# Kernel optimization log

Hardware: AMD Instinct MI355X
Metric: run time of the kernel (lower is better)

Reference implementation:

```python
import jax, jax.numpy as jnp
import numpy as np

N_NODES = 100000
N_EDGES = 1600000
D = 64
N_LAYERS = 5


def setup_inputs() -> dict:
    key = jax.random.key(0)
    k1, k2, k3, k4 = jax.random.split(key, 4)
    x = jax.random.normal(k1, (N_NODES, D), dtype=jnp.float32)
    edge_index = jax.random.randint(k2, (2, N_EDGES), 0, N_NODES, dtype=jnp.int32)
    scale = 1.0 / np.sqrt(D)
    Wl = jax.random.normal(k3, (N_LAYERS, D, D), dtype=jnp.float32) * scale
    Wr = jax.random.normal(k4, (N_LAYERS, D, D), dtype=jnp.float32) * scale
    b = jnp.zeros((N_LAYERS, D), dtype=jnp.float32)
    return {"x": x, "edge_index": edge_index, "Wl": Wl, "Wr": Wr, "b": b}


def reference(x, edge_index, Wl, Wr, b):
    # PyG SAGEConv (mean aggr): out = lin_l(mean_{j->i} x_j) + lin_r(x_i)
    # bias lives on lin_l; messages flow src=edge_index[0] -> dst=edge_index[1].
    src = edge_index[0]
    dst = edge_index[1]
    n = x.shape[0]
    deg = jax.ops.segment_sum(jnp.ones((src.shape[0],), x.dtype), dst, num_segments=n)
    inv_deg = (1.0 / jnp.maximum(deg, 1.0))[:, None]  # [N,1]

    def conv(h, i):
        agg = jax.ops.segment_sum(h[src], dst, num_segments=n) * inv_deg  # [N,D] mean of neighbors
        return agg @ Wl[i] + b[i] + h @ Wr[i]

    # first num_layers-1 convs with relu (+ residual for i>0); dropout is identity in eval mode
    for i in range(N_LAYERS - 1):
        prev = x
        x = conv(x, i)
        if i > 0:
            x = x + prev
        x = jax.nn.relu(x)
    return conv(x, N_LAYERS - 1)
```

## Files before the change

### kernel.cpp

```cpp
#include <hip/hip_runtime.h>

#define DIM 64
#define SCAN_CHUNK 1024


__global__ void zero_int_kernel(int* __restrict__ p, int n) {
    int i = blockIdx.x * blockDim.x + threadIdx.x;
    if (i < n) p[i] = 0;
}

__global__ void deg_kernel(const int* __restrict__ dst, int* __restrict__ deg, int n_edges) {
    int i = blockIdx.x * blockDim.x + threadIdx.x;
    int e0 = i * 4;
    if (e0 + 3 < n_edges) {
        int4 d4 = *(const int4*)(dst + e0);
        atomicAdd(&deg[d4.x], 1);
        atomicAdd(&deg[d4.y], 1);
        atomicAdd(&deg[d4.z], 1);
        atomicAdd(&deg[d4.w], 1);
    } else {
        for (int e = e0; e < n_edges; ++e) atomicAdd(&deg[dst[e]], 1);
    }
}

__global__ void bsum_kernel(const int* __restrict__ deg, int* __restrict__ bsum, int n) {
    int t = threadIdx.x;
    int base = blockIdx.x * SCAN_CHUNK;
    int s = 0;
    #pragma unroll
    for (int k = 0; k < 4; ++k) {
        int i = base + t + k * 256;
        if (i < n) s += deg[i];
    }
    __shared__ int red[4];
    #pragma unroll
    for (int off = 32; off > 0; off >>= 1) s += __shfl_down(s, off);
    if ((t & 63) == 0) red[t >> 6] = s;
    __syncthreads();
    if (t == 0) bsum[blockIdx.x] = red[0] + red[1] + red[2] + red[3];
}

__global__ void bscan_kernel(int* __restrict__ bsum, int nb, int* __restrict__ row_ofs, int n) {
    __shared__ int lds[256];
    int t = threadIdx.x;
    int v = (t < nb) ? bsum[t] : 0;
    lds[t] = v;
    __syncthreads();
    #pragma unroll
    for (int off = 1; off < 256; off <<= 1) {
        int u = (t >= off) ? lds[t - off] : 0;
        __syncthreads();
        lds[t] += u;
        __syncthreads();
    }
    if (t < nb) bsum[t] = lds[t] - v;
    if (t == nb - 1) row_ofs[n] = lds[t];
}

__global__ void chunk_scan_kernel(const int* __restrict__ deg, const int* __restrict__ bsum,
                                  int* __restrict__ row_ofs, int* __restrict__ cursor,
                                  float* __restrict__ inv_deg, int n) {
    __shared__ int lds[256];
    int t = threadIdx.x;
    int base = blockIdx.x * SCAN_CHUNK + t * 4;
    int v[4];
    int s = 0;
    #pragma unroll
    for (int k = 0; k < 4; ++k) {
        int i = base + k;
        v[k] = (i < n) ? deg[i] : 0;
        s += v[k];
    }
    lds[t] = s;
    __syncthreads();
    #pragma unroll
    for (int off = 1; off < 256; off <<= 1) {
        int u = (t >= off) ? lds[t - off] : 0;
        __syncthreads();
        lds[t] += u;
        __syncthreads();
    }
    int excl = lds[t] - s + bsum[blockIdx.x];
    #pragma unroll
    for (int k = 0; k < 4; ++k) {
        int i = base + k;
        if (i < n) {
            row_ofs[i] = excl;
            cursor[i]  = excl;
            inv_deg[i] = 1.0f / fmaxf((float)v[k], 1.0f);
        }
        excl += v[k];
    }
}

__global__ void fill_kernel(const int* __restrict__ src, const int* __restrict__ dst,
                            int* __restrict__ cursor, int* __restrict__ csr_src, int n_edges) {
    int i = blockIdx.x * blockDim.x + threadIdx.x;
    int e0 = i * 4;
    if (e0 + 3 < n_edges) {
        int4 s4 = *(const int4*)(src + e0);
        int4 d4 = *(const int4*)(dst + e0);
        csr_src[atomicAdd(&cursor[d4.x], 1)] = s4.x;
        csr_src[atomicAdd(&cursor[d4.y], 1)] = s4.y;
        csr_src[atomicAdd(&cursor[d4.z], 1)] = s4.z;
        csr_src[atomicAdd(&cursor[d4.w], 1)] = s4.w;
    } else {
        for (int e = e0; e < n_edges; ++e)
            csr_src[atomicAdd(&cursor[dst[e]], 1)] = src[e];
    }
}

__global__ __launch_bounds__(256) void agg_kernel_v1(
    const float* __restrict__ h, const int* __restrict__ row_ofs,
    const int* __restrict__ csr, const float* __restrict__ invd,
    float* __restrict__ agg, int n) {
    const int lane = threadIdx.x & 63;
    const int nw = (gridDim.x * blockDim.x) >> 6;
    int wave0 = (blockIdx.x * blockDim.x + threadIdx.x) >> 6;

    for (int nid = wave0; nid < n; nid += nw) {
        const int s = __builtin_amdgcn_readfirstlane(row_ofs[nid]);
        const int e = __builtin_amdgcn_readfirstlane(row_ofs[nid + 1]);
        const float iv = invd[nid];
        float a0 = 0.f, a1 = 0.f, a2 = 0.f, a3 = 0.f;
        float a4 = 0.f, a5 = 0.f, a6 = 0.f, a7 = 0.f;
        for (int c = s; c < e; c += 64) {
            int rem = e - c;
            int cnt = rem < 64 ? rem : 64;
            int vi = (lane < cnt) ? csr[c + lane] : 0;
            int t = 0;
            for (; t + 8 <= cnt; t += 8) {
                int i0 = __builtin_amdgcn_readlane(vi, t);
                int i1 = __builtin_amdgcn_readlane(vi, t + 1);
                int i2 = __builtin_amdgcn_readlane(vi, t + 2);
                int i3 = __builtin_amdgcn_readlane(vi, t + 3);
                int i4 = __builtin_amdgcn_readlane(vi, t + 4);
                int i5 = __builtin_amdgcn_readlane(vi, t + 5);
                int i6 = __builtin_amdgcn_readlane(vi, t + 6);
                int i7 = __builtin_amdgcn_readlane(vi, t + 7);
                a0 += h[(size_t)i0 * DIM + lane];
                a1 += h[(size_t)i1 * DIM + lane];
                a2 += h[(size_t)i2 * DIM + lane];
                a3 += h[(size_t)i3 * DIM + lane];
                a4 += h[(size_t)i4 * DIM + lane];
                a5 += h[(size_t)i5 * DIM + lane];
                a6 += h[(size_t)i6 * DIM + lane];
                a7 += h[(size_t)i7 * DIM + lane];
            }
            for (; t + 4 <= cnt; t += 4) {
                int i0 = __builtin_amdgcn_readlane(vi, t);
                int i1 = __builtin_amdgcn_readlane(vi, t + 1);
                int i2 = __builtin_amdgcn_readlane(vi, t + 2);
                int i3 = __builtin_amdgcn_readlane(vi, t + 3);
                a0 += h[(size_t)i0 * DIM + lane];
                a1 += h[(size_t)i1 * DIM + lane];
                a2 += h[(size_t)i2 * DIM + lane];
                a3 += h[(size_t)i3 * DIM + lane];
            }
            for (; t < cnt; ++t)
                a0 += h[(size_t)__builtin_amdgcn_readlane(vi, t) * DIM + lane];
        }
        float r = ((a0 + a1) + (a2 + a3)) + ((a4 + a5) + (a6 + a7));
        agg[(size_t)nid * DIM + lane] = r * iv;
    }
}

__global__ __launch_bounds__(256) void agg_kernel_v2(
    const float* __restrict__ h, const int* __restrict__ row_ofs,
    const int* __restrict__ csr, const float* __restrict__ invd,
    float* __restrict__ agg, int n) {
    const int lane = threadIdx.x & 63;
    const int g = lane >> 4;
    const int q = lane & 15;
    const int nw = (gridDim.x * blockDim.x) >> 6;
    int wave0 = (blockIdx.x * blockDim.x + threadIdx.x) >> 6;

    for (int nid = wave0; nid < n; nid += nw) {
        const int s = __builtin_amdgcn_readfirstlane(row_ofs[nid]);
        const int e = __builtin_amdgcn_readfirstlane(row_ofs[nid + 1]);
        float4 acc0 = make_float4(0.f, 0.f, 0.f, 0.f);
        float4 acc1 = make_float4(0.f, 0.f, 0.f, 0.f);
        for (int c = s; c < e; c += 64) {
            int rem = e - c;
            int cnt = rem < 64 ? rem : 64;
            int vi = (lane < cnt) ? csr[c + lane] : 0;
            for (int t = 0; t < cnt; t += 8) {
                int r0 = t + g;
                int r1 = t + 4 + g;
                int cl = cnt - 1;
                int i0 = __shfl(vi, r0 < cl ? r0 : cl);
                int i1 = __shfl(vi, r1 < cl ? r1 : cl);
                float4 v0 = *(const float4*)(h + (size_t)i0 * DIM + q * 4);
                float4 v1 = *(const float4*)(h + (size_t)i1 * DIM + q * 4);
                float f0 = (r0 < cnt) ? 1.f : 0.f;
                float f1 = (r1 < cnt) ? 1.f : 0.f;
                acc0.x = fmaf(v0.x, f0, acc0.x);
                acc0.y = fmaf(v0.y, f0, acc0.y);
                acc0.z = fmaf(v0.z, f0, acc0.z);
                acc0.w = fmaf(v0.w, f0, acc0.w);
                acc1.x = fmaf(v1.x, f1, acc1.x);
                acc1.y = fmaf(v1.y, f1, acc1.y);
                acc1.z = fmaf(v1.z, f1, acc1.z);
                acc1.w = fmaf(v1.w, f1, acc1.w);
            }
        }
        float4 r;
        r.x = acc0.x + acc1.x;
        r.y = acc0.y + acc1.y;
        r.z = acc0.z + acc1.z;
        r.w = acc0.w + acc1.w;
        r.x += __shfl_xor(r.x, 16);
        r.y += __shfl_xor(r.y, 16);
        r.z += __shfl_xor(r.z, 16);
        r.w += __shfl_xor(r.w, 16);
        r.x += __shfl_xor(r.x, 32);
        r.y += __shfl_xor(r.y, 32);
        r.z += __shfl_xor(r.z, 32);
        r.w += __shfl_xor(r.w, 32);
        const float iv = invd[nid];
        if (lane < 16) {
            float4 o = make_float4(r.x * iv, r.y * iv, r.z * iv, r.w * iv);
            *(float4*)(agg + (size_t)nid * DIM + q * 4) = o;
        }
    }
}

__global__ __launch_bounds__(256, 1) void transform_kernel(
    const float* __restrict__ agg, const float* __restrict__ h,
    const float* __restrict__ Wl, const float* __restrict__ Wr,
    const float* __restrict__ bias, float* __restrict__ out,
    int n, int resid, int relu) {
    const int lane = threadIdx.x & 63;

    float wl[DIM], wr[DIM];
    #pragma unroll
    for (int d = 0; d < DIM; ++d) {
        wl[d] = Wl[d * DIM + lane];
        wr[d] = Wr[d * DIM + lane];
    }
    const float bv = bias[lane];

    const int nw = (gridDim.x * blockDim.x) >> 6;
    int nid = (blockIdx.x * blockDim.x + threadIdx.x) >> 6;
    if (nid >= n) return;

    float av = agg[(size_t)nid * DIM + lane];
    float hv = h[(size_t)nid * DIM + lane];

    while (true) {
        int nxt = nid + nw;
        float avn = 0.f, hvn = 0.f;
        if (nxt < n) {
            avn = agg[(size_t)nxt * DIM + lane];
            hvn = h[(size_t)nxt * DIM + lane];
        }
        float o0 = bv, o1 = 0.f, o2 = 0.f, o3 = 0.f;
        #pragma unroll
        for (int d = 0; d < DIM; d += 2) {
            float ad0 = __int_as_float(__builtin_amdgcn_readlane(__float_as_int(av), d));
            float hd0 = __int_as_float(__builtin_amdgcn_readlane(__float_as_int(hv), d));
            float ad1 = __int_as_float(__builtin_amdgcn_readlane(__float_as_int(av), d + 1));
            float hd1 = __int_as_float(__builtin_amdgcn_readlane(__float_as_int(hv), d + 1));
            o0 += ad0 * wl[d];
            o1 += hd0 * wr[d];
            o2 += ad1 * wl[d + 1];
            o3 += hd1 * wr[d + 1];
        }
        float o = (o0 + o2) + (o1 + o3);
        if (resid) o += hv;
        if (relu) o = fmaxf(o, 0.f);
        out[(size_t)nid * DIM + lane] = o;
        if (nxt >= n) break;
        nid = nxt;
        av = avn;
        hv = hvn;
    }
}


extern "C" void kernel_launch(void* const* d_in, const int* in_sizes, int n_in,
                              void* d_out, int out_size, void* d_ws, size_t ws_size,
                              hipStream_t stream) {
    const float* x  = (const float*)d_in[0];
    const int*   ei = (const int*)d_in[1];
    const float* Wl = (const float*)d_in[2];
    const float* Wr = (const float*)d_in[3];
    const float* b  = (const float*)d_in[4];

    int N = in_sizes[0] / DIM;
    int E = in_sizes[1] / 2;
    int L = in_sizes[2] / (DIM * DIM);
    const int* src = ei;
    const int* dst = ei + E;
    float* out_f = (float*)d_out;

    char* w = (char*)d_ws;
    size_t o = 0;
    auto carve = [&](size_t bytes) {
        void* p = w + o;
        o = (o + bytes + 255) & ~(size_t)255;
        return p;
    };
    float* aggb    = (float*)carve((size_t)N * DIM * 4);
    float* hB      = (float*)carve((size_t)N * DIM * 4);
    int*   deg     = (int*)carve((size_t)N * 4);
    int*   row_ofs = (int*)carve((size_t)(N + 1) * 4);
    int*   cursor  = (int*)carve((size_t)N * 4);
    float* invd    = (float*)carve((size_t)N * 4);
    int*   csr     = (int*)carve((size_t)E * 4);
    int    nb      = (N + SCAN_CHUNK - 1) / SCAN_CHUNK;
    int*   bsum    = (int*)carve((size_t)nb * 4);

    zero_int_kernel<<<(N + 255) / 256, 256, 0, stream>>>(deg, N);
    deg_kernel<<<(E / 4 + 255) / 256, 256, 0, stream>>>(dst, deg, E);
    bsum_kernel<<<nb, 256, 0, stream>>>(deg, bsum, N);
    bscan_kernel<<<1, 256, 0, stream>>>(bsum, nb, row_ofs, N);
    chunk_scan_kernel<<<nb, 256, 0, stream>>>(deg, bsum, row_ofs, cursor, invd, N);
    fill_kernel<<<(E / 4 + 255) / 256, 256, 0, stream>>>(src, dst, cursor, csr, E);

    const float* hcur = x;
    for (int i = 0; i < L; ++i) {
        if (i & 1)
            agg_kernel_v2<<<4096, 256, 0, stream>>>(hcur, row_ofs, csr, invd, aggb, N);
        else
            agg_kernel_v1<<<4096, 256, 0, stream>>>(hcur, row_ofs, csr, invd, aggb, N);

        int relu  = (i < L - 1) ? 1 : 0;
        int resid = (i > 0 && i < L - 1) ? 1 : 0;
        float* outp;
        if (i == L - 1) {
            outp = (hcur != out_f) ? out_f : hB;
        } else {
            outp = (hcur == out_f) ? hB : out_f;
        }
        transform_kernel<<<1024, 256, 0, stream>>>(
            aggb, hcur, Wl + (size_t)i * DIM * DIM, Wr + (size_t)i * DIM * DIM,
            b + (size_t)i * DIM, outp, N, resid, relu);

        if (i == L - 1 && outp != out_f)
            hipMemcpyAsync(out_f, outp, (size_t)N * DIM * 4,
                           hipMemcpyDeviceToDevice, stream);
        hcur = outp;
    }
}
```

Before: 801.3 us.

## Shard degree count and CSR fill atomics by destination range

The degree-count and CSR fill kernels now run with blocks assigned to one of 8 destination-node shards. Each block scans a chunk of edges and only does atomics for destinations in its shard, so atomics and scattered writes stay within a smaller address range with better L2 locality. The cost is that every edge index is read 8 times, which adds global read traffic.

```diff
diff --git a/kernel.cpp b/kernel.cpp
--- a/kernel.cpp
+++ b/kernel.cpp
@@ -2,6 +2,8 @@
 
 #define DIM 64
 #define SCAN_CHUNK 1024
+#define NSHARD 8
+#define FILL_CHUNKS 512
 
 
 __global__ void zero_int_kernel(int* __restrict__ p, int n) {
@@ -9,17 +11,30 @@
     if (i < n) p[i] = 0;
 }
 
-__global__ void deg_kernel(const int* __restrict__ dst, int* __restrict__ deg, int n_edges) {
-    int i = blockIdx.x * blockDim.x + threadIdx.x;
-    int e0 = i * 4;
-    if (e0 + 3 < n_edges) {
-        int4 d4 = *(const int4*)(dst + e0);
-        atomicAdd(&deg[d4.x], 1);
-        atomicAdd(&deg[d4.y], 1);
-        atomicAdd(&deg[d4.z], 1);
-        atomicAdd(&deg[d4.w], 1);
-    } else {
-        for (int e = e0; e < n_edges; ++e) atomicAdd(&deg[dst[e]], 1);
+__global__ __launch_bounds__(256) void deg_kernel_sharded(
+    const int* __restrict__ dst, int* __restrict__ deg, int n_edges, int shard_sz) {
+    const int shard = blockIdx.x & (NSHARD - 1);
+    const int lo = shard * shard_sz;
+    const int hi = lo + shard_sz;
+    const int nch = gridDim.x >> 3;
+    const int ch = blockIdx.x >> 3;
+    long per = ((long)n_edges + nch - 1) / nch;
+    per = (per + 3) & ~3L;
+    const long e0 = (long)ch * per;
+    const long e1 = (e0 + per < (long)n_edges) ? e0 + per : (long)n_edges;
+    for (long b = e0 + (long)threadIdx.x * 4; b < e1; b += 256 * 4) {
+        if (b + 3 < e1) {
+            int4 d4 = *(const int4*)(dst + b);
+            if (d4.x >= lo && d4.x < hi) atomicAdd(&deg[d4.x], 1);
+            if (d4.y >= lo && d4.y < hi) atomicAdd(&deg[d4.y], 1);
+            if (d4.z >= lo && d4.z < hi) atomicAdd(&deg[d4.z], 1);
+            if (d4.w >= lo && d4.w < hi) atomicAdd(&deg[d4.w], 1);
+        } else {
+            for (long e = b; e < e1; ++e) {
+                int d = dst[e];
+                if (d >= lo && d < hi) atomicAdd(&deg[d], 1);
+            }
+        }
     }
 }
 
@@ -93,20 +108,32 @@
     }
 }
 
-__global__ void fill_kernel(const int* __restrict__ src, const int* __restrict__ dst,
-                            int* __restrict__ cursor, int* __restrict__ csr_src, int n_edges) {
-    int i = blockIdx.x * blockDim.x + threadIdx.x;
-    int e0 = i * 4;
-    if (e0 + 3 < n_edges) {
-        int4 s4 = *(const int4*)(src + e0);
-        int4 d4 = *(const int4*)(dst + e0);
-        csr_src[atomicAdd(&cursor[d4.x], 1)] = s4.x;
-        csr_src[atomicAdd(&cursor[d4.y], 1)] = s4.y;
-        csr_src[atomicAdd(&cursor[d4.z], 1)] = s4.z;
-        csr_src[atomicAdd(&cursor[d4.w], 1)] = s4.w;
-    } else {
-        for (int e = e0; e < n_edges; ++e)
-            csr_src[atomicAdd(&cursor[dst[e]], 1)] = src[e];
+__global__ __launch_bounds__(256) void fill_kernel_sharded(
+    const int* __restrict__ src, const int* __restrict__ dst,
+    int* __restrict__ cursor, int* __restrict__ csr_src, int n_edges, int shard_sz) {
+    const int shard = blockIdx.x & (NSHARD - 1);
+    const int lo = shard * shard_sz;
+    const int hi = lo + shard_sz;
+    const int nch = gridDim.x >> 3;
+    const int ch = blockIdx.x >> 3;
+    long per = ((long)n_edges + nch - 1) / nch;
+    per = (per + 3) & ~3L;
+    const long e0 = (long)ch * per;
+    const long e1 = (e0 + per < (long)n_edges) ? e0 + per : (long)n_edges;
+    for (long b = e0 + (long)threadIdx.x * 4; b < e1; b += 256 * 4) {
+        if (b + 3 < e1) {
+            int4 s4 = *(const int4*)(src + b);
+            int4 d4 = *(const int4*)(dst + b);
+            if (d4.x >= lo && d4.x < hi) csr_src[atomicAdd(&cursor[d4.x], 1)] = s4.x;
+            if (d4.y >= lo && d4.y < hi) csr_src[atomicAdd(&cursor[d4.y], 1)] = s4.y;
+            if (d4.z >= lo && d4.z < hi) csr_src[atomicAdd(&cursor[d4.z], 1)] = s4.z;
+            if (d4.w >= lo && d4.w < hi) csr_src[atomicAdd(&cursor[d4.w], 1)] = s4.w;
+        } else {
+            for (long e = b; e < e1; ++e) {
+                int d = dst[e];
+                if (d >= lo && d < hi) csr_src[atomicAdd(&cursor[d], 1)] = src[e];
+            }
+        }
     }
 }
 
@@ -311,12 +338,14 @@
     int    nb      = (N + SCAN_CHUNK - 1) / SCAN_CHUNK;
     int*   bsum    = (int*)carve((size_t)nb * 4);
 
+    int shard_sz = (N + NSHARD - 1) / NSHARD;
+
     zero_int_kernel<<<(N + 255) / 256, 256, 0, stream>>>(deg, N);
-    deg_kernel<<<(E / 4 + 255) / 256, 256, 0, stream>>>(dst, deg, E);
+    deg_kernel_sharded<<<FILL_CHUNKS * NSHARD, 256, 0, stream>>>(dst, deg, E, shard_sz);
     bsum_kernel<<<nb, 256, 0, stream>>>(deg, bsum, N);
     bscan_kernel<<<1, 256, 0, stream>>>(bsum, nb, row_ofs, N);
     chunk_scan_kernel<<<nb, 256, 0, stream>>>(deg, bsum, row_ofs, cursor, invd, N);
-    fill_kernel<<<(E / 4 + 255) / 256, 256, 0, stream>>>(src, dst, cursor, csr, E);
+    fill_kernel_sharded<<<FILL_CHUNKS * NSHARD, 256, 0, stream>>>(src, dst, cursor, csr, E, shard_sz);
 
     const float* hcur = x;
     for (int i = 0; i < L; ++i) {
@@ -338,8 +367,8 @@
             b + (size_t)i * DIM, outp, N, resid, relu);
 
         if (i == L - 1 && outp != out_f)
-            hipMemcpyAsync(out_f, outp, (size_t)N * DIM * 4,
-                           hipMemcpyDeviceToDevice, stream);
+            (void)hipMemcpyAsync(out_f, outp, (size_t)N * DIM * 4,
+                                 hipMemcpyDeviceToDevice, stream);
         hcur = outp;
     }
 }
```

Result: faster. 751.5 us (-6.2%).

## Bucket edges by destination shard before degree count and CSR fill

Applied to the files above, without the earlier changes.

Adds a partition pass that groups edges into 8 destination-range shards using wave-level ballot aggregation. The degree-count and CSR-fill kernels then read the bucketed edges, so their atomics target a narrower node range for better cache locality. This costs an extra read and write pass over all edges, plus fixed-capacity buckets that assume a roughly balanced destination distribution.

```diff
diff --git a/kernel.cpp b/kernel.cpp
--- a/kernel.cpp
+++ b/kernel.cpp
@@ -2,25 +2,60 @@
 
 #define DIM 64
 #define SCAN_CHUNK 1024
-
-
-__global__ void zero_int_kernel(int* __restrict__ p, int n) {
+#define NSHARD 8
+
+
+__global__ void zero2_kernel(int* __restrict__ p, int n, int* __restrict__ q, int m) {
     int i = blockIdx.x * blockDim.x + threadIdx.x;
     if (i < n) p[i] = 0;
-}
-
-__global__ void deg_kernel(const int* __restrict__ dst, int* __restrict__ deg, int n_edges) {
-    int i = blockIdx.x * blockDim.x + threadIdx.x;
-    int e0 = i * 4;
-    if (e0 + 3 < n_edges) {
-        int4 d4 = *(const int4*)(dst + e0);
-        atomicAdd(&deg[d4.x], 1);
-        atomicAdd(&deg[d4.y], 1);
-        atomicAdd(&deg[d4.z], 1);
-        atomicAdd(&deg[d4.w], 1);
-    } else {
-        for (int e = e0; e < n_edges; ++e) atomicAdd(&deg[dst[e]], 1);
-    }
+    if (i < m) q[i] = 0;
+}
+
+__global__ __launch_bounds__(256) void partition_kernel(
+    const int* __restrict__ src, const int* __restrict__ dst, int n_edges,
+    int shard_sz, int* __restrict__ bcnt,
+    int* __restrict__ bsrc, int* __restrict__ bdst, int cap) {
+    const int lane = threadIdx.x & 63;
+    const long stride = (long)gridDim.x * blockDim.x;
+    long wbase = (long)blockIdx.x * blockDim.x + (threadIdx.x & ~63);
+    for (; wbase < n_edges; wbase += stride) {
+        long e = wbase + lane;
+        bool valid = e < n_edges;
+        int d = valid ? dst[e] : 0;
+        int s = valid ? src[e] : 0;
+        int sh = valid ? (d / shard_sz) : -1;
+        #pragma unroll
+        for (int k = 0; k < NSHARD; ++k) {
+            unsigned long long m = __ballot(sh == k);
+            if (m == 0ull) continue;
+            int cnt = __popcll(m);
+            int leader = __ffsll((long long)m) - 1;
+            int bidx = 0;
+            if (lane == leader) bidx = atomicAdd(&bcnt[k], cnt);
+            bidx = __shfl(bidx, leader);
+            if (sh == k) {
+                int my = __popcll(m & ((1ull << lane) - 1ull));
+                int pos = k * cap + bidx + my;
+                bsrc[pos] = s;
+                bdst[pos] = d;
+            }
+        }
+    }
+}
+
+__global__ __launch_bounds__(256) void deg_bucket_kernel(
+    const int* __restrict__ bdst, const int* __restrict__ bcnt,
+    int* __restrict__ deg, int cap) {
+    const int shard = blockIdx.x & (NSHARD - 1);
+    const int nch = gridDim.x >> 3;
+    const int ch = blockIdx.x >> 3;
+    const int cnt = bcnt[shard];
+    const int per = (cnt + nch - 1) / nch;
+    const int s0 = ch * per;
+    const int s1 = (s0 + per < cnt) ? s0 + per : cnt;
+    const int* p = bdst + (size_t)shard * cap;
+    for (int i = s0 + threadIdx.x; i < s1; i += 256)
+        atomicAdd(&deg[p[i]], 1);
 }
 
 __global__ void bsum_kernel(const int* __restrict__ deg, int* __restrict__ bsum, int n) {
@@ -93,20 +128,22 @@
     }
 }
 
-__global__ void fill_kernel(const int* __restrict__ src, const int* __restrict__ dst,
-                            int* __restrict__ cursor, int* __restrict__ csr_src, int n_edges) {
-    int i = blockIdx.x * blockDim.x + threadIdx.x;
-    int e0 = i * 4;
-    if (e0 + 3 < n_edges) {
-        int4 s4 = *(const int4*)(src + e0);
-        int4 d4 = *(const int4*)(dst + e0);
-        csr_src[atomicAdd(&cursor[d4.x], 1)] = s4.x;
-        csr_src[atomicAdd(&cursor[d4.y], 1)] = s4.y;
-        csr_src[atomicAdd(&cursor[d4.z], 1)] = s4.z;
-        csr_src[atomicAdd(&cursor[d4.w], 1)] = s4.w;
-    } else {
-        for (int e = e0; e < n_edges; ++e)
-            csr_src[atomicAdd(&cursor[dst[e]], 1)] = src[e];
+__global__ __launch_bounds__(256) void fill_bucket_kernel(
+    const int* __restrict__ bsrc, const int* __restrict__ bdst,
+    const int* __restrict__ bcnt, int* __restrict__ cursor,
+    int* __restrict__ csr_src, int cap) {
+    const int shard = blockIdx.x & (NSHARD - 1);
+    const int nch = gridDim.x >> 3;
+    const int ch = blockIdx.x >> 3;
+    const int cnt = bcnt[shard];
+    const int per = (cnt + nch - 1) / nch;
+    const int s0 = ch * per;
+    const int s1 = (s0 + per < cnt) ? s0 + per : cnt;
+    const int* ps = bsrc + (size_t)shard * cap;
+    const int* pd = bdst + (size_t)shard * cap;
+    for (int i = s0 + threadIdx.x; i < s1; i += 256) {
+        int d = pd[i];
+        csr_src[atomicAdd(&cursor[d], 1)] = ps[i];
     }
 }
 
@@ -310,13 +347,20 @@
     int*   csr     = (int*)carve((size_t)E * 4);
     int    nb      = (N + SCAN_CHUNK - 1) / SCAN_CHUNK;
     int*   bsum    = (int*)carve((size_t)nb * 4);
-
-    zero_int_kernel<<<(N + 255) / 256, 256, 0, stream>>>(deg, N);
-    deg_kernel<<<(E / 4 + 255) / 256, 256, 0, stream>>>(dst, deg, E);
+    int    cap     = E / NSHARD + E / (NSHARD * 4) + 1024;
+    int*   bsrc    = (int*)carve((size_t)NSHARD * cap * 4);
+    int*   bdst    = (int*)carve((size_t)NSHARD * cap * 4);
+    int*   bcnt    = (int*)carve((size_t)NSHARD * 4);
+
+    int shard_sz = (N + NSHARD - 1) / NSHARD;
+
+    zero2_kernel<<<(N + 255) / 256, 256, 0, stream>>>(deg, N, bcnt, NSHARD);
+    partition_kernel<<<2048, 256, 0, stream>>>(src, dst, E, shard_sz, bcnt, bsrc, bdst, cap);
+    deg_bucket_kernel<<<256 * NSHARD, 256, 0, stream>>>(bdst, bcnt, deg, cap);
     bsum_kernel<<<nb, 256, 0, stream>>>(deg, bsum, N);
     bscan_kernel<<<1, 256, 0, stream>>>(bsum, nb, row_ofs, N);
     chunk_scan_kernel<<<nb, 256, 0, stream>>>(deg, bsum, row_ofs, cursor, invd, N);
-    fill_kernel<<<(E / 4 + 255) / 256, 256, 0, stream>>>(src, dst, cursor, csr, E);
+    fill_bucket_kernel<<<256 * NSHARD, 256, 0, stream>>>(bsrc, bdst, bcnt, cursor, csr, cap);
 
     const float* hcur = x;
     for (int i = 0; i < L; ++i) {
@@ -338,8 +382,8 @@
             b + (size_t)i * DIM, outp, N, resid, relu);
 
         if (i == L - 1 && outp != out_f)
-            hipMemcpyAsync(out_f, outp, (size_t)N * DIM * 4,
-                           hipMemcpyDeviceToDevice, stream);
+            (void)hipMemcpyAsync(out_f, outp, (size_t)N * DIM * 4,
+                                 hipMemcpyDeviceToDevice, stream);
         hcur = outp;
     }
 }
```

Result: slower. 3.023 ms (+277.3%).
